# Optimization experiments

Hardware: AMD Instinct MI355X
Metric: run time of the kernel (lower is better)

The kernel has to match this reference:

```python
import jax, jax.numpy as jnp
import numpy as np

B, S, D = 8, 2048, 1024

def setup_inputs() -> dict:
    key = jax.random.key(0)
    kq, kk, kv = jax.random.split(key, 3)
    qm = jax.random.normal(kq, (B, S, D), dtype=jnp.float32)
    km = jax.random.normal(kk, (B, S, D), dtype=jnp.float32)
    vm = jax.random.normal(kv, (B, S, D), dtype=jnp.float32)
    return {"qm": qm, "km": km, "vm": vm}

def reference(qm, km, vm):
    # qkm = qm @ km^T / sqrt(d_k)   -> [B, S, S]
    scale = 1.0 / jnp.sqrt(jnp.asarray(qm.shape[-1], dtype=qm.dtype))
    qkm = jnp.einsum('bqd,bkd->bqk', qm, km) * scale
    # NOTE: faithful to source: softmax is applied AFTER the second matmul,
    # i.e. softmax((QK^T/sqrt(d)) @ V, axis=-1). masking=False (module default).
    out = jnp.einsum('bqk,bkd->bqd', qkm, vm)  # [B, S, D]
    return jax.nn.softmax(out, axis=-1)
```

## Files before the change

### kernel.cpp

```cpp
#include <hip/hip_runtime.h>
#include <hip/hip_bf16.h>
#include <stdint.h>

#define BATCH 8
#define SEQ   2048
#define DIM   1024

typedef unsigned short u16;
typedef __attribute__((ext_vector_type(8))) short short8;
typedef __attribute__((ext_vector_type(4))) float f32x4;
typedef __attribute__((ext_vector_type(4))) unsigned short us4;

__device__ __forceinline__ u16 f2bf(float x){
  union { float f; uint32_t u; } c; c.f = x;
  uint32_t u = c.u;
  uint32_t r = u + 0x7fffu + ((u >> 16) & 1u);
  return (u16)(r >> 16);
}
__device__ __forceinline__ float bf2f(u16 s){
  union { uint32_t u; float f; } c; c.u = ((uint32_t)s) << 16;
  return c.f;
}

__device__ __forceinline__ void gload16(const void* g, void* l){
  __builtin_amdgcn_global_load_lds(
      (const __attribute__((address_space(1))) void*)g,
      (__attribute__((address_space(3))) void*)l, 16, 0, 0);
}

__global__ __launch_bounds__(256) void k_split(const float* __restrict__ src,
                                               u16* __restrict__ dst, int nchunk){
  for (int i = blockIdx.x*blockDim.x + threadIdx.x; i < nchunk; i += gridDim.x*blockDim.x){
    int r = i >> 8;
    int c = (i & 255) << 2;
    f32x4 v = *(const f32x4*)(src + (size_t)r*DIM + c);
    us4 h, l;
    #pragma unroll
    for (int j = 0; j < 4; j++){
      u16 hh = f2bf(v[j]);
      h[j] = hh;
      l[j] = f2bf(v[j] - bf2f(hh));
    }
    u16* d = dst + (size_t)r*(2*DIM) + c;
    *(us4*)d         = h;
    *(us4*)(d + DIM) = l;
  }
}

__global__ __launch_bounds__(256) void k_convert_vt(const float* __restrict__ V,
                                                    u16* __restrict__ Vts){
  __shared__ float tile[32][33];
  int z = blockIdx.z;
  const float* Vb = V + (size_t)z * SEQ * DIM;
  u16* Vtb = Vts + (size_t)z * DIM * (2*SEQ);
  int s0 = blockIdx.x * 32, d0 = blockIdx.y * 32;
  int tx = threadIdx.x, ty = threadIdx.y;
  #pragma unroll
  for (int i = 0; i < 4; i++){
    tile[ty + i*8][tx] = Vb[(size_t)(s0 + ty + i*8) * DIM + d0 + tx];
  }
  __syncthreads();
  #pragma unroll
  for (int i = 0; i < 4; i++){
    int dr = ty + i*8;
    float x = tile[tx][dr];
    u16 h = f2bf(x);
    u16 l = f2bf(x - bf2f(h));
    size_t off = (size_t)(d0 + dr) * (2*SEQ) + s0 + tx;
    Vtb[off]       = h;
    Vtb[off + SEQ] = l;
  }
}

template<int N_, int KB, int SPLITOUT, int BX, int RX, int RY>
__global__ __launch_bounds__(256,2) void k_gemm(const u16* __restrict__ A,
                                                const u16* __restrict__ B,
                                                void* __restrict__ Cout,
                                                size_t aStride, size_t bStride, size_t cStride){
  constexpr int LA = 2*KB;
  __shared__ __align__(16) u16 Ah[128*64], Al[128*64], Bh[128*64], Bl[128*64];

  int orig = blockIdx.x;
  int xcd = orig & 7;
  int idx = orig >> 3;
  constexpr int RN = RX * RY;
  int z  = idx / RN;
  int r  = idx % RN;
  int bx = (xcd % (BX/RX)) * RX + (r % RX);
  int by = (xcd / (BX/RX)) * RY + (r / RX);

  const u16* Ab = A + (size_t)z * aStride;
  const u16* Bb = B + (size_t)z * bStride;

  int t = threadIdx.x, lane = t & 63, w = t >> 6;
  int wm = (w & 1) * 64, wn = (w >> 1) * 64;
  int fr = lane & 15;

  int srow    = lane >> 3;
  int srcSlot = ((lane & 7) ^ (lane >> 3)) * 8;

  const u16* aBase = Ab + ((size_t)bx*128) * LA + srcSlot;
  const u16* bBase = Bb + ((size_t)by*128) * LA + srcSlot;

  int rdSlot0 = (((0*4) + (lane >> 4)) ^ (lane & 7)) * 8;
  int rdSlot1 = (((1*4) + (lane >> 4)) ^ (lane & 7)) * 8;

  f32x4 acc[4][4] = {};

  for (int k0 = 0; k0 < KB; k0 += 64){
    #pragma unroll
    for (int j = 0; j < 4; j++){
      int c = w*4 + j;
      size_t rOff = (size_t)(c*8 + srow) * LA + k0;
      const u16* ga = aBase + rOff;
      const u16* gb = bBase + rOff;
      int le = c * 512;
      gload16(ga,      Ah + le);
      gload16(ga + KB, Al + le);
      gload16(gb,      Bh + le);
      gload16(gb + KB, Bl + le);
    }
    __syncthreads();

    #pragma unroll
    for (int ksub = 0; ksub < 2; ksub++){
      int rs = ksub ? rdSlot1 : rdSlot0;
      short8 fah[4], fal[4], fbh[4], fbl[4];
      #pragma unroll
      for (int mi = 0; mi < 4; mi++){
        fah[mi] = *(const short8*)&Ah[(wm + mi*16 + fr)*64 + rs];
        fal[mi] = *(const short8*)&Al[(wm + mi*16 + fr)*64 + rs];
        fbh[mi] = *(const short8*)&Bh[(wn + mi*16 + fr)*64 + rs];
        fbl[mi] = *(const short8*)&Bl[(wn + mi*16 + fr)*64 + rs];
      }
      #pragma unroll
      for (int mi = 0; mi < 4; mi++){
        #pragma unroll
        for (int ni = 0; ni < 4; ni++){
          acc[mi][ni] = __builtin_amdgcn_mfma_f32_16x16x32_bf16(fah[mi], fbh[ni], acc[mi][ni], 0,0,0);
          acc[mi][ni] = __builtin_amdgcn_mfma_f32_16x16x32_bf16(fah[mi], fbl[ni], acc[mi][ni], 0,0,0);
          acc[mi][ni] = __builtin_amdgcn_mfma_f32_16x16x32_bf16(fal[mi], fbh[ni], acc[mi][ni], 0,0,0);
        }
      }
    }
    __syncthreads();
  }

  int cr = (lane >> 4) * 4, cc = lane & 15;
  if (SPLITOUT){
    u16* Cb = (u16*)Cout + (size_t)z * cStride;
    const float scale = 0.03125f;
    #pragma unroll
    for (int mi = 0; mi < 4; mi++){
      int gr = bx*128 + wm + mi*16 + cr;
      #pragma unroll
      for (int ni = 0; ni < 4; ni++){
        int gc = by*128 + wn + ni*16 + cc;
        #pragma unroll
        for (int rr = 0; rr < 4; rr++){
          float x = acc[mi][ni][rr] * scale;
          u16 h = f2bf(x);
          u16 l = f2bf(x - bf2f(h));
          size_t off = (size_t)(gr + rr) * (2*N_) + gc;
          Cb[off]      = h;
          Cb[off + N_] = l;
        }
      }
    }
  } else {
    float* Cb = (float*)Cout + (size_t)z * cStride;
    #pragma unroll
    for (int mi = 0; mi < 4; mi++){
      int gr = bx*128 + wm + mi*16 + cr;
      #pragma unroll
      for (int ni = 0; ni < 4; ni++){
        int gc = by*128 + wn + ni*16 + cc;
        #pragma unroll
        for (int rr = 0; rr < 4; rr++){
          Cb[(size_t)(gr + rr) * N_ + gc] = acc[mi][ni][rr];
        }
      }
    }
  }
}

__global__ __launch_bounds__(256) void k_softmax(float* __restrict__ O){
  float* p = O + (size_t)blockIdx.x * DIM;
  int t = threadIdx.x;
  int lane = t & 63, wave = t >> 6;
  f32x4 v = *(f32x4*)(p + t*4);
  float m = fmaxf(fmaxf(v[0], v[1]), fmaxf(v[2], v[3]));
  #pragma unroll
  for (int o = 32; o > 0; o >>= 1) m = fmaxf(m, __shfl_xor(m, o));
  __shared__ float rmax[4], rsum[4];
  if (lane == 0) rmax[wave] = m;
  __syncthreads();
  m = fmaxf(fmaxf(rmax[0], rmax[1]), fmaxf(rmax[2], rmax[3]));
  float e0 = expf(v[0]-m), e1 = expf(v[1]-m), e2 = expf(v[2]-m), e3 = expf(v[3]-m);
  float s = e0 + e1 + e2 + e3;
  #pragma unroll
  for (int o = 32; o > 0; o >>= 1) s += __shfl_xor(s, o);
  if (lane == 0) rsum[wave] = s;
  __syncthreads();
  s = rsum[0] + rsum[1] + rsum[2] + rsum[3];
  float inv = 1.0f / s;
  f32x4 rv = { e0*inv, e1*inv, e2*inv, e3*inv };
  *(f32x4*)(p + t*4) = rv;
}

extern "C" void kernel_launch(void* const* d_in, const int* in_sizes, int n_in,
                              void* d_out, int out_size, void* d_ws, size_t ws_size,
                              hipStream_t stream){
  const float* Q = (const float*)d_in[0];
  const float* K = (const float*)d_in[1];
  const float* V = (const float*)d_in[2];
  float* Out = (float*)d_out;
  u16* w = (u16*)d_ws;

  const size_t QsB = (size_t)SEQ * (2*DIM);
  const size_t KtB = (size_t)DIM * (2*SEQ);
  const size_t VtB = KtB;
  const size_t WsB = (size_t)DIM * (2*DIM);

  dim3 blk(256);
  dim3 cblk(32, 8);

  const size_t need1 = 8 * (QsB + KtB + VtB + WsB) * sizeof(u16);
  const size_t need2 = 8 * (KtB + VtB + WsB) * sizeof(u16);

  if (ws_size >= need1){
    u16* Qs = w;
    u16* Kt = Qs + 8*QsB;
    u16* Vt = Kt + 8*KtB;
    u16* Ws = Vt + 8*VtB;
    k_split<<<dim3(2048), blk, 0, stream>>>(Q, Qs, 8*SEQ*(DIM/4));
    k_convert_vt<<<dim3(SEQ/32, DIM/32, 8), cblk, 0, stream>>>(K, Kt);
    k_convert_vt<<<dim3(SEQ/32, DIM/32, 8), cblk, 0, stream>>>(V, Vt);
    k_gemm<DIM, SEQ, 1, 8, 2, 4><<<dim3(512), blk, 0, stream>>>(Vt, Kt, Ws, VtB, KtB, WsB);
    k_gemm<DIM, DIM, 0, 16, 4, 4><<<dim3(1024), blk, 0, stream>>>(Qs, Ws, Out, QsB, WsB, (size_t)SEQ*DIM);
  } else if (ws_size >= need2){
    u16* Kt = w;
    u16* Vt = Kt + 8*KtB;
    u16* Ws = Vt + 8*VtB;
    u16* Qs = w;
    k_convert_vt<<<dim3(SEQ/32, DIM/32, 8), cblk, 0, stream>>>(K, Kt);
    k_convert_vt<<<dim3(SEQ/32, DIM/32, 8), cblk, 0, stream>>>(V, Vt);
    k_gemm<DIM, SEQ, 1, 8, 2, 4><<<dim3(512), blk, 0, stream>>>(Vt, Kt, Ws, VtB, KtB, WsB);
    k_split<<<dim3(2048), blk, 0, stream>>>(Q, Qs, 8*SEQ*(DIM/4));
    k_gemm<DIM, DIM, 0, 16, 4, 4><<<dim3(1024), blk, 0, stream>>>(Qs, Ws, Out, QsB, WsB, (size_t)SEQ*DIM);
  } else {
    u16* Qs = w;
    u16* Kt = Qs + QsB;
    u16* Vt = Kt + KtB;
    u16* Ws = Vt + VtB;
    for (int b = 0; b < BATCH; b++){
      const size_t inOff = (size_t)b * SEQ * DIM;
      k_split<<<dim3(1024), blk, 0, stream>>>(Q + inOff, Qs, SEQ*(DIM/4));
      k_convert_vt<<<dim3(SEQ/32, DIM/32, 1), cblk, 0, stream>>>(K + inOff, Kt);
      k_convert_vt<<<dim3(SEQ/32, DIM/32, 1), cblk, 0, stream>>>(V + inOff, Vt);
      k_gemm<DIM, SEQ, 1, 8, 2, 4><<<dim3(64), blk, 0, stream>>>(Vt, Kt, Ws, VtB, KtB, WsB);
      k_gemm<DIM, DIM, 0, 16, 4, 4><<<dim3(128), blk, 0, stream>>>(Qs, Ws, Out + inOff, QsB, WsB, (size_t)SEQ*DIM);
    }
  }
  k_softmax<<<dim3(BATCH*SEQ), blk, 0, stream>>>(Out);
}
```

Baseline: 312.3 us.

## Double-buffer GEMM LDS loads and vectorize transpose-convert kernel

The GEMM main loop now uses two LDS buffers, prefetching the next K-slab with async global-to-LDS loads while computing on the current one, synchronized with explicit vmcnt waits and barriers. This doubles LDS use to 128KB, so launch bounds drop to one block per CU. The K/V transpose-convert kernel moves to 64x64 tiles with float4 global loads and 4-wide bf16 stores to reduce memory transaction count. The risk is lower occupancy and reliance on a hand-picked vmcnt value matching the number of loads issued.

```diff
diff --git a/kernel.cpp b/kernel.cpp
--- a/kernel.cpp
+++ b/kernel.cpp
@@ -49,36 +49,48 @@
 
 __global__ __launch_bounds__(256) void k_convert_vt(const float* __restrict__ V,
                                                     u16* __restrict__ Vts){
-  __shared__ float tile[32][33];
+  __shared__ float tile[64][65];
   int z = blockIdx.z;
   const float* Vb = V + (size_t)z * SEQ * DIM;
   u16* Vtb = Vts + (size_t)z * DIM * (2*SEQ);
-  int s0 = blockIdx.x * 32, d0 = blockIdx.y * 32;
-  int tx = threadIdx.x, ty = threadIdx.y;
+  int s0 = blockIdx.x * 64, d0 = blockIdx.y * 64;
+  int t = threadIdx.x;
+  int rs = t >> 4;
+  int cd = (t & 15) * 4;
   #pragma unroll
   for (int i = 0; i < 4; i++){
-    tile[ty + i*8][tx] = Vb[(size_t)(s0 + ty + i*8) * DIM + d0 + tx];
+    int s = rs + i*16;
+    f32x4 v = *(const f32x4*)(Vb + (size_t)(s0 + s)*DIM + d0 + cd);
+    tile[s][cd+0] = v[0]; tile[s][cd+1] = v[1];
+    tile[s][cd+2] = v[2]; tile[s][cd+3] = v[3];
   }
   __syncthreads();
+  int dl = t >> 4;
+  int sl = (t & 15) * 4;
   #pragma unroll
   for (int i = 0; i < 4; i++){
-    int dr = ty + i*8;
-    float x = tile[tx][dr];
-    u16 h = f2bf(x);
-    u16 l = f2bf(x - bf2f(h));
-    size_t off = (size_t)(d0 + dr) * (2*SEQ) + s0 + tx;
-    Vtb[off]       = h;
-    Vtb[off + SEQ] = l;
+    int d = dl + i*16;
+    us4 h, l;
+    #pragma unroll
+    for (int j = 0; j < 4; j++){
+      float x = tile[sl+j][d];
+      u16 hh = f2bf(x);
+      h[j] = hh;
+      l[j] = f2bf(x - bf2f(hh));
+    }
+    size_t off = (size_t)(d0 + d) * (2*SEQ) + s0 + sl;
+    *(us4*)(Vtb + off)       = h;
+    *(us4*)(Vtb + off + SEQ) = l;
   }
 }
 
 template<int N_, int KB, int SPLITOUT, int BX, int RX, int RY>
-__global__ __launch_bounds__(256,2) void k_gemm(const u16* __restrict__ A,
+__global__ __launch_bounds__(256,1) void k_gemm(const u16* __restrict__ A,
                                                 const u16* __restrict__ B,
                                                 void* __restrict__ Cout,
                                                 size_t aStride, size_t bStride, size_t cStride){
   constexpr int LA = 2*KB;
-  __shared__ __align__(16) u16 Ah[128*64], Al[128*64], Bh[128*64], Bl[128*64];
+  __shared__ __align__(16) u16 lds[2][4][128*64];
 
   int orig = blockIdx.x;
   int xcd = orig & 7;
@@ -107,44 +119,62 @@
 
   f32x4 acc[4][4] = {};
 
-  for (int k0 = 0; k0 < KB; k0 += 64){
-    #pragma unroll
-    for (int j = 0; j < 4; j++){
-      int c = w*4 + j;
-      size_t rOff = (size_t)(c*8 + srow) * LA + k0;
-      const u16* ga = aBase + rOff;
-      const u16* gb = bBase + rOff;
-      int le = c * 512;
-      gload16(ga,      Ah + le);
-      gload16(ga + KB, Al + le);
-      gload16(gb,      Bh + le);
-      gload16(gb + KB, Bl + le);
-    }
-    __syncthreads();
-
-    #pragma unroll
-    for (int ksub = 0; ksub < 2; ksub++){
-      int rs = ksub ? rdSlot1 : rdSlot0;
-      short8 fah[4], fal[4], fbh[4], fbl[4];
-      #pragma unroll
-      for (int mi = 0; mi < 4; mi++){
-        fah[mi] = *(const short8*)&Ah[(wm + mi*16 + fr)*64 + rs];
-        fal[mi] = *(const short8*)&Al[(wm + mi*16 + fr)*64 + rs];
-        fbh[mi] = *(const short8*)&Bh[(wn + mi*16 + fr)*64 + rs];
-        fbl[mi] = *(const short8*)&Bl[(wn + mi*16 + fr)*64 + rs];
-      }
-      #pragma unroll
-      for (int mi = 0; mi < 4; mi++){
-        #pragma unroll
-        for (int ni = 0; ni < 4; ni++){
-          acc[mi][ni] = __builtin_amdgcn_mfma_f32_16x16x32_bf16(fah[mi], fbh[ni], acc[mi][ni], 0,0,0);
-          acc[mi][ni] = __builtin_amdgcn_mfma_f32_16x16x32_bf16(fah[mi], fbl[ni], acc[mi][ni], 0,0,0);
-          acc[mi][ni] = __builtin_amdgcn_mfma_f32_16x16x32_bf16(fal[mi], fbh[ni], acc[mi][ni], 0,0,0);
-        }
-      }
-    }
-    __syncthreads();
-  }
+  #define STAGE(buf, k0)                                                      \
+    { _Pragma("unroll")                                                       \
+      for (int j = 0; j < 4; j++){                                            \
+        int c = w*4 + j;                                                      \
+        size_t rOff = (size_t)(c*8 + srow) * LA + (k0);                       \
+        const u16* ga = aBase + rOff;                                         \
+        const u16* gb = bBase + rOff;                                         \
+        int le = c * 512;                                                     \
+        gload16(ga,      &lds[buf][0][le]);                                   \
+        gload16(ga + KB, &lds[buf][1][le]);                                   \
+        gload16(gb,      &lds[buf][2][le]);                                   \
+        gload16(gb + KB, &lds[buf][3][le]);                                   \
+      } }
+
+  #define COMPUTE(buf)                                                        \
+    { _Pragma("unroll")                                                       \
+      for (int ksub = 0; ksub < 2; ksub++){                                   \
+        int rs = ksub ? rdSlot1 : rdSlot0;                                    \
+        short8 fah[4], fal[4], fbh[4], fbl[4];                                \
+        _Pragma("unroll")                                                     \
+        for (int mi = 0; mi < 4; mi++){                                       \
+          fah[mi] = *(const short8*)&lds[buf][0][(wm + mi*16 + fr)*64 + rs];  \
+          fal[mi] = *(const short8*)&lds[buf][1][(wm + mi*16 + fr)*64 + rs];  \
+          fbh[mi] = *(const short8*)&lds[buf][2][(wn + mi*16 + fr)*64 + rs];  \
+          fbl[mi] = *(const short8*)&lds[buf][3][(wn + mi*16 + fr)*64 + rs];  \
+        }                                                                     \
+        _Pragma("unroll")                                                     \
+        for (int mi = 0; mi < 4; mi++){                                       \
+          _Pragma("unroll")                                                   \
+          for (int ni = 0; ni < 4; ni++){                                     \
+            acc[mi][ni] = __builtin_amdgcn_mfma_f32_16x16x32_bf16(fah[mi], fbh[ni], acc[mi][ni], 0,0,0); \
+            acc[mi][ni] = __builtin_amdgcn_mfma_f32_16x16x32_bf16(fah[mi], fbl[ni], acc[mi][ni], 0,0,0); \
+            acc[mi][ni] = __builtin_amdgcn_mfma_f32_16x16x32_bf16(fal[mi], fbh[ni], acc[mi][ni], 0,0,0); \
+          }                                                                   \
+        } } }
+
+  STAGE(0, 0)
+  int cur = 0;
+  for (int k0 = 0; k0 + 64 < KB; k0 += 64, cur ^= 1){
+    STAGE(cur^1, k0 + 64)
+    asm volatile("s_waitcnt vmcnt(16)" ::: "memory");
+    __builtin_amdgcn_sched_barrier(0);
+    __builtin_amdgcn_s_barrier();
+    __builtin_amdgcn_sched_barrier(0);
+    COMPUTE(cur)
+    __builtin_amdgcn_sched_barrier(0);
+    __builtin_amdgcn_s_barrier();
+  }
+  asm volatile("s_waitcnt vmcnt(0)" ::: "memory");
+  __builtin_amdgcn_sched_barrier(0);
+  __builtin_amdgcn_s_barrier();
+  __builtin_amdgcn_sched_barrier(0);
+  COMPUTE(cur)
+
+  #undef STAGE
+  #undef COMPUTE
 
   int cr = (lane >> 4) * 4, cc = lane & 15;
   if (SPLITOUT){
@@ -223,7 +253,7 @@
   const size_t WsB = (size_t)DIM * (2*DIM);
 
   dim3 blk(256);
-  dim3 cblk(32, 8);
+  dim3 cgrid(SEQ/64, DIM/64, 8);
 
   const size_t need1 = 8 * (QsB + KtB + VtB + WsB) * sizeof(u16);
   const size_t need2 = 8 * (KtB + VtB + WsB) * sizeof(u16);
@@ -234,8 +264,8 @@
     u16* Vt = Kt + 8*KtB;
     u16* Ws = Vt + 8*VtB;
     k_split<<<dim3(2048), blk, 0, stream>>>(Q, Qs, 8*SEQ*(DIM/4));
-    k_convert_vt<<<dim3(SEQ/32, DIM/32, 8), cblk, 0, stream>>>(K, Kt);
-    k_convert_vt<<<dim3(SEQ/32, DIM/32, 8), cblk, 0, stream>>>(V, Vt);
+    k_convert_vt<<<cgrid, blk, 0, stream>>>(K, Kt);
+    k_convert_vt<<<cgrid, blk, 0, stream>>>(V, Vt);
     k_gemm<DIM, SEQ, 1, 8, 2, 4><<<dim3(512), blk, 0, stream>>>(Vt, Kt, Ws, VtB, KtB, WsB);
     k_gemm<DIM, DIM, 0, 16, 4, 4><<<dim3(1024), blk, 0, stream>>>(Qs, Ws, Out, QsB, WsB, (size_t)SEQ*DIM);
   } else if (ws_size >= need2){
@@ -243,8 +273,8 @@
     u16* Vt = Kt + 8*KtB;
     u16* Ws = Vt + 8*VtB;
     u16* Qs = w;
-    k_convert_vt<<<dim3(SEQ/32, DIM/32, 8), cblk, 0, stream>>>(K, Kt);
-    k_convert_vt<<<dim3(SEQ/32, DIM/32, 8), cblk, 0, stream>>>(V, Vt);
+    k_convert_vt<<<cgrid, blk, 0, stream>>>(K, Kt);
+    k_convert_vt<<<cgrid, blk, 0, stream>>>(V, Vt);
     k_gemm<DIM, SEQ, 1, 8, 2, 4><<<dim3(512), blk, 0, stream>>>(Vt, Kt, Ws, VtB, KtB, WsB);
     k_split<<<dim3(2048), blk, 0, stream>>>(Q, Qs, 8*SEQ*(DIM/4));
     k_gemm<DIM, DIM, 0, 16, 4, 4><<<dim3(1024), blk, 0, stream>>>(Qs, Ws, Out, QsB, WsB, (size_t)SEQ*DIM);
@@ -253,11 +283,12 @@
     u16* Kt = Qs + QsB;
     u16* Vt = Kt + KtB;
     u16* Ws = Vt + VtB;
+    dim3 cg1(SEQ/64, DIM/64, 1);
     for (int b = 0; b < BATCH; b++){
       const size_t inOff = (size_t)b * SEQ * DIM;
       k_split<<<dim3(1024), blk, 0, stream>>>(Q + inOff, Qs, SEQ*(DIM/4));
-      k_convert_vt<<<dim3(SEQ/32, DIM/32, 1), cblk, 0, stream>>>(K + inOff, Kt);
-      k_convert_vt<<<dim3(SEQ/32, DIM/32, 1), cblk, 0, stream>>>(V + inOff, Vt);
+      k_convert_vt<<<cg1, blk, 0, stream>>>(K + inOff, Kt);
+      k_convert_vt<<<cg1, blk, 0, stream>>>(V + inOff, Vt);
       k_gemm<DIM, SEQ, 1, 8, 2, 4><<<dim3(64), blk, 0, stream>>>(Vt, Kt, Ws, VtB, KtB, WsB);
       k_gemm<DIM, DIM, 0, 16, 4, 4><<<dim3(128), blk, 0, stream>>>(Qs, Ws, Out + inOff, QsB, WsB, (size_t)SEQ*DIM);
     }
```

Result: slower. 357.0 us (+14.3%).
